# Optimization experiments

Measured on AMD Instinct MI355X. Metric: run time of the kernel, lower is better.

Reference implementation:

```python
import jax, jax.numpy as jnp
import numpy as np

B, C, N, H = 4, 256, 2048, 8
D = C // 4  # q/k projection dim
BN_EPS = 1e-5


def setup_inputs() -> dict:
    key = jax.random.key(0)
    ks = jax.random.split(key, 16)
    s = lambda fan: 1.0 / np.sqrt(fan)
    return {
        "x": jax.random.normal(ks[0], (B, C, N), dtype=jnp.float32),
        # per-head params, stacked on leading head axis
        "w_qk": jax.random.normal(ks[1], (H, D, C), dtype=jnp.float32) * s(C),  # shared q/k conv weight
        "w_v": jax.random.normal(ks[2], (H, C, C), dtype=jnp.float32) * s(C),
        "b_v": jax.random.normal(ks[3], (H, C), dtype=jnp.float32) * 0.01,
        "w_t": jax.random.normal(ks[4], (H, C, C), dtype=jnp.float32) * s(C),
        "b_t": jax.random.normal(ks[5], (H, C), dtype=jnp.float32) * 0.01,
        "bn_g": jnp.ones((H, C), dtype=jnp.float32),
        "bn_b": jnp.zeros((H, C), dtype=jnp.float32),
        "bn_m": jax.random.normal(ks[6], (H, C), dtype=jnp.float32) * 0.1,
        "bn_v": jax.random.uniform(ks[7], (H, C), dtype=jnp.float32, minval=0.5, maxval=1.5),
        # final 1x1 conv + BN (LeakyReLU 0.2)
        "w_lin": jax.random.normal(ks[8], (C, C * H), dtype=jnp.float32) * s(C * H),
        "lbn_g": jnp.ones((C,), dtype=jnp.float32),
        "lbn_b": jnp.zeros((C,), dtype=jnp.float32),
        "lbn_m": jax.random.normal(ks[9], (C,), dtype=jnp.float32) * 0.1,
        "lbn_v": jax.random.uniform(ks[10], (C,), dtype=jnp.float32, minval=0.5, maxval=1.5),
    }


def _oa_head(x, w_qk, w_v, b_v, w_t, b_t, g, b, m, v):
    # x: [B, C, N]; 1x1 Conv1d == channel matmul
    x_q = jnp.einsum("dc,bcn->bnd", w_qk, x)                 # [B, N, D]
    x_k = jnp.einsum("dc,bcn->bdn", w_qk, x)                 # [B, D, N] (shared weight)
    x_v = jnp.einsum("ec,bcn->ben", w_v, x) + b_v[:, None]   # [B, C, N]
    energy = jnp.einsum("bnd,bdm->bnm", x_q, x_k)            # [B, N, N]
    attn = jax.nn.softmax(energy, axis=-1)
    attn = attn / (1e-9 + attn.sum(axis=1, keepdims=True))   # extra L1 renorm over dim=1
    x_r = jnp.einsum("ben,bnm->bem", x_v, attn)              # [B, C, N]
    y = jnp.einsum("ec,bcn->ben", w_t, x - x_r) + b_t[:, None]
    y = (y - m[:, None]) * (g[:, None] / jnp.sqrt(v[:, None] + BN_EPS)) + b[:, None]
    return x + jax.nn.relu(y)


def reference(x, w_qk, w_v, b_v, w_t, b_t, bn_g, bn_b, bn_m, bn_v,
              w_lin, lbn_g, lbn_b, lbn_m, lbn_v):
    # run all H heads via vmap over stacked params -> [B, H, C, N]
    heads = jax.vmap(_oa_head, in_axes=(None, 0, 0, 0, 0, 0, 0, 0, 0, 0), out_axes=1)(
        x, w_qk, w_v, b_v, w_t, b_t, bn_g, bn_b, bn_m, bn_v)
    cat = heads.reshape(x.shape[0], H * C, x.shape[2])       # torch.cat(dim=1) order
    y = jnp.einsum("ck,bkn->bcn", w_lin, cat)                # 1x1 conv, no bias
    y = (y - lbn_m[:, None]) * (lbn_g[:, None] / jnp.sqrt(lbn_v[:, None] + BN_EPS)) + lbn_b[:, None]
    return jnp.where(y >= 0, y, 0.2 * y)                     # LeakyReLU(0.2)
```

## Files before the change

### kernel.cpp

```cpp
#include <hip/hip_runtime.h>
#include <math.h>

#define B_ 4
#define C_ 256
#define N_ 2048
#define H_ 8
#define D_ 64
#define BH_ 32
#define HC_ 2048
#define BN_EPS 1e-5f
#define SCL 1.2011224087864498f

typedef __attribute__((ext_vector_type(8))) short s8v;
typedef __attribute__((ext_vector_type(4))) short s4v;
typedef __attribute__((ext_vector_type(8))) _Float16 h8v;
typedef __attribute__((ext_vector_type(4))) _Float16 h4v;
typedef __attribute__((ext_vector_type(4))) float f32x4;

#define MFMA __builtin_amdgcn_mfma_f32_16x16x32_bf16
#define MFMAH __builtin_amdgcn_mfma_f32_16x16x32_f16

static __device__ __forceinline__ unsigned short f2b(float f) {
  union { float f; unsigned int i; } v; v.f = f;
  unsigned int r = v.i + 0x7FFFu + ((v.i >> 16) & 1u);
  return (unsigned short)(r >> 16);
}
static __device__ __forceinline__ float fexp2(float x) {
  float r;
  asm("v_exp_f32 %0, %1" : "=v"(r) : "v"(x));
  return r;
}
static __device__ __forceinline__ unsigned cvtpk(float lo, float hi) {
  unsigned r;
  asm("v_cvt_pk_bf16_f32 %0, %1, %2" : "=v"(r) : "v"(lo), "v"(hi));
  return r;
}
static __device__ __forceinline__ void gload16(const void* g, void* l) {
  __builtin_amdgcn_global_load_lds(
      (const __attribute__((address_space(1))) unsigned int*)g,
      (__attribute__((address_space(3))) unsigned int*)l, 16, 0, 0);
}

struct GP {
  const float *x, *w_qk, *w_v, *b_v, *w_t, *b_t, *bn_g, *bn_b, *bn_m, *bn_v;
  const float *w_lin, *lbn_g, *lbn_b, *lbn_m, *lbn_v;
  _Float16 *PT, *xT, *wqk16, *wvh;
  short *HOT, *wtb, *wlinb, *Vb, *xmr;
  float *part, *shb, *nrm, *sh, *out;
};

__global__ __launch_bounds__(256) void cvt_k(const float* __restrict__ in,
                                             short* __restrict__ out) {
  int i = (blockIdx.x * 256 + threadIdx.x) * 4;
  float4 v = *(const float4*)(in + i);
  s4v o = { (short)f2b(v.x), (short)f2b(v.y), (short)f2b(v.z), (short)f2b(v.w) };
  *(s4v*)(out + i) = o;
}

__global__ __launch_bounds__(256) void cvth_k(const float* __restrict__ in,
                                              _Float16* __restrict__ out) {
  int i = (blockIdx.x * 256 + threadIdx.x) * 4;
  float4 v = *(const float4*)(in + i);
  h4v o = { (_Float16)v.x, (_Float16)v.y, (_Float16)v.z, (_Float16)v.w };
  *(h4v*)(out + i) = o;
}

__global__ __launch_bounds__(256) void xcvt_k(const float* __restrict__ x,
                                              _Float16* __restrict__ xT) {
  const int n0 = blockIdx.x * 64, c0 = blockIdx.y * 64, b = blockIdx.z;
  const float* xb = x + (size_t)b * C_ * N_;
  __shared__ float sm[64][65];
  const int t = threadIdx.x;
#pragma unroll
  for (int i = 0; i < 4; ++i) {
    int idx = i * 256 + t;
    int c = idx >> 4, j = (idx & 15) * 4;
    float4 v = *(const float4*)(xb + (size_t)(c0 + c) * N_ + n0 + j);
    sm[j + 0][c] = v.x; sm[j + 1][c] = v.y; sm[j + 2][c] = v.z; sm[j + 3][c] = v.w;
  }
  __syncthreads();
#pragma unroll
  for (int i = 0; i < 2; ++i) {
    int idx = i * 256 + t;
    int n = idx >> 3, cg = (idx & 7) * 8;
    h8v o;
#pragma unroll
    for (int d = 0; d < 8; ++d) o[d] = (_Float16)sm[n][cg + d];
    *(h8v*)(xT + ((size_t)b * N_ + n0 + n) * C_ + c0 + cg) = o;
  }
}

__global__ __launch_bounds__(256, 2) void p_k(GP p) {
  const int t = threadIdx.x, wv = t >> 6, lane = t & 63;
  const int l15 = lane & 15, l4 = lane >> 4;
  const int n0 = blockIdx.x * 128;
  const int bh = blockIdx.y, b = bh / H_, h = bh % H_;
  const _Float16* Ag = p.wqk16 + h * D_ * C_;
  const _Float16* Bg = p.xT + (size_t)b * N_ * C_;
  __shared__ _Float16 As[64 * 64], Bs[128 * 64];
  __shared__ float Tr[128 * 65];
  f32x4 acc[4][2] = {};
  for (int kc = 0; kc < 256; kc += 64) {
    __syncthreads();
#pragma unroll
    for (int i = 0; i < 2; ++i) {
      int idx = i * 256 + t;
      int row = idx >> 3, offl = (idx & 7) * 16;
      gload16((const char*)(Ag + (size_t)row * C_ + kc) + (offl ^ ((row & 7) << 4)),
              (char*)As + idx * 16);
    }
#pragma unroll
    for (int i = 0; i < 4; ++i) {
      int idx = i * 256 + t;
      int row = idx >> 3, offl = (idx & 7) * 16;
      gload16((const char*)(Bg + (size_t)(n0 + row) * C_ + kc) + (offl ^ ((row & 7) << 4)),
              (char*)Bs + idx * 16);
    }
    __syncthreads();
    h8v ad[4][2], bn[2][2];
#pragma unroll
    for (int d = 0; d < 4; ++d)
#pragma unroll
      for (int ks = 0; ks < 2; ++ks) {
        int row = d * 16 + l15;
        ad[d][ks] = *(const h8v*)((const char*)As + row * 128 + ((ks * 64 + l4 * 16) ^ ((row & 7) << 4)));
      }
#pragma unroll
    for (int nb = 0; nb < 2; ++nb)
#pragma unroll
      for (int ks = 0; ks < 2; ++ks) {
        int row = wv * 32 + nb * 16 + l15;
        bn[nb][ks] = *(const h8v*)((const char*)Bs + row * 128 + ((ks * 64 + l4 * 16) ^ ((row & 7) << 4)));
      }
#pragma unroll
    for (int d = 0; d < 4; ++d)
#pragma unroll
      for (int nb = 0; nb < 2; ++nb) {
        acc[d][nb] = MFMAH(ad[d][0], bn[nb][0], acc[d][nb], 0, 0, 0);
        acc[d][nb] = MFMAH(ad[d][1], bn[nb][1], acc[d][nb], 0, 0, 0);
      }
  }
  __syncthreads();
#pragma unroll
  for (int d = 0; d < 4; ++d)
#pragma unroll
    for (int nb = 0; nb < 2; ++nb)
#pragma unroll
      for (int r = 0; r < 4; ++r) {
        int n_l = wv * 32 + nb * 16 + l15;
        int dd = d * 16 + l4 * 4 + r;
        Tr[n_l * 65 + dd] = acc[d][nb][r];
      }
  __syncthreads();
  _Float16* Pf = p.PT + ((size_t)bh * N_ + n0) * D_;
  float* nz = p.nrm + (size_t)bh * N_;
#pragma unroll
  for (int i = 0; i < 4; ++i) {
    int idx = i * 256 + t;
    int n = idx >> 3, dg = (idx & 7) * 8;
    h8v hv;
    float ssq = 0.f;
#pragma unroll
    for (int j = 0; j < 8; ++j) {
      float v = Tr[n * 65 + dg + j] * SCL;
      ssq = fmaf(v, v, ssq);
      hv[j] = (_Float16)v;
    }
    *(h8v*)(Pf + (size_t)n * D_ + dg) = hv;
    ssq += __shfl_xor(ssq, 1, 64);
    ssq += __shfl_xor(ssq, 2, 64);
    ssq += __shfl_xor(ssq, 4, 64);
    if ((t & 7) == 0) nz[n0 + n] = ssq;
  }
}

__global__ __launch_bounds__(256) void shift_k(const float* __restrict__ nrm,
                                               float* __restrict__ sh) {
  const int z = blockIdx.x, t = threadIdx.x;
  const float* nz = nrm + (size_t)z * N_;
  float loc[8];
  float mx = 0.f;
#pragma unroll
  for (int i = 0; i < 8; ++i) {
    loc[i] = nz[i * 256 + t];
    mx = fmaxf(mx, loc[i]);
  }
  for (int o = 32; o; o >>= 1) mx = fmaxf(mx, __shfl_xor(mx, o, 64));
  __shared__ float sb[4];
  if ((t & 63) == 0) sb[t >> 6] = mx;
  __syncthreads();
  float M = sqrtf(fmaxf(fmaxf(sb[0], sb[1]), fmaxf(sb[2], sb[3])));
#pragma unroll
  for (int i = 0; i < 8; ++i)
    sh[(size_t)z * N_ + i * 256 + t] = sqrtf(loc[i]) * M;
}

__global__ __launch_bounds__(256, 4) void passa_k(GP p) {
  const int t = threadIdx.x, wv = t >> 6, lane = t & 63;
  const int l15 = lane & 15, l4 = lane >> 4;
  const int wr = wv >> 1, wc = wv & 1;
  const int z = blockIdx.x;
  int idx = blockIdx.y;
  int ti = 0;
  while (idx >= 16 - ti) { idx -= 16 - ti; ++ti; }
  const int tj = ti + idx;
  const int r0 = ti * 128, c0 = tj * 128;
  const _Float16* Pz = p.PT + (size_t)z * N_ * D_;
  const float* shz = p.sh + (size_t)z * N_;
  __shared__ short RH[8192], CH[8192];
  __shared__ float rbuf[2][2][64], cbuf[2][2][64];
#pragma unroll
  for (int i = 0; i < 4; ++i) {
    int c2 = i * 256 + t;
    int row = c2 >> 3, offl = (c2 & 7) * 16;
    int so = offl ^ ((row & 7) << 4);
    gload16((const char*)(Pz + (size_t)(r0 + row) * D_) + so, (char*)RH + c2 * 16);
    if (ti != tj)
      gload16((const char*)(Pz + (size_t)(c0 + row) * D_) + so, (char*)CH + c2 * 16);
  }
  __syncthreads();
  const char* BHp = (ti == tj) ? (const char*)RH : (const char*)CH;

  h8v bh4[4][2];
  float shc[4];
#pragma unroll
  for (int nf = 0; nf < 4; ++nf) {
#pragma unroll
    for (int ks = 0; ks < 2; ++ks) {
      int row = wc * 64 + nf * 16 + l15;
      int byte = row * 128 + ((ks * 64 + l4 * 16) ^ ((row & 7) << 4));
      bh4[nf][ks] = *(const h8v*)(BHp + byte);
    }
    shc[nf] = shz[c0 + wc * 64 + nf * 16 + l15];
  }
  float rowp[4][4] = {};
  float colp[4] = {};
#pragma unroll
  for (int mf = 0; mf < 4; ++mf) {
    h8v ah[2];
#pragma unroll
    for (int ks = 0; ks < 2; ++ks) {
      int row = wr * 64 + mf * 16 + l15;
      int byte = row * 128 + ((ks * 64 + l4 * 16) ^ ((row & 7) << 4));
      ah[ks] = *(const h8v*)((const char*)RH + byte);
    }
    f32x4 shr = *(const f32x4*)(shz + r0 + wr * 64 + mf * 16 + l4 * 4);
#pragma unroll
    for (int nf = 0; nf < 4; ++nf) {
      f32x4 s = {};
      s = MFMAH(ah[0], bh4[nf][0], s, 0, 0, 0);
      s = MFMAH(ah[1], bh4[nf][1], s, 0, 0, 0);
      rowp[mf][0] += fexp2(s[0] - shr[0]);
      rowp[mf][1] += fexp2(s[1] - shr[1]);
      rowp[mf][2] += fexp2(s[2] - shr[2]);
      rowp[mf][3] += fexp2(s[3] - shr[3]);
      if (ti != tj)
        colp[nf] += fexp2(s[0] - shc[nf]) + fexp2(s[1] - shc[nf]) +
                    fexp2(s[2] - shc[nf]) + fexp2(s[3] - shc[nf]);
    }
  }
#pragma unroll
  for (int mf = 0; mf < 4; ++mf)
#pragma unroll
    for (int r = 0; r < 4; ++r) {
      float v = rowp[mf][r];
      v += __shfl_xor(v, 1, 64); v += __shfl_xor(v, 2, 64);
      v += __shfl_xor(v, 4, 64); v += __shfl_xor(v, 8, 64);
      rowp[mf][r] = v;
    }
#pragma unroll
  for (int nf = 0; nf < 4; ++nf) {
    float v = colp[nf];
    v += __shfl_xor(v, 16, 64); v += __shfl_xor(v, 32, 64);
    colp[nf] = v;
  }
  if (l15 == 0)
#pragma unroll
    for (int mf = 0; mf < 4; ++mf)
#pragma unroll
      for (int r = 0; r < 4; ++r)
        rbuf[wr][wc][mf * 16 + l4 * 4 + r] = rowp[mf][r];
  if (l4 == 0)
#pragma unroll
    for (int nf = 0; nf < 4; ++nf)
      cbuf[wc][wr][nf * 16 + l15] = colp[nf];
  __syncthreads();
  if (t < 128) {
    float v = rbuf[t >> 6][0][t & 63] + rbuf[t >> 6][1][t & 63];
    p.part[((size_t)z * 16 + tj) * N_ + r0 + t] = v;
  } else if (ti != tj) {
    int u = t - 128;
    float v = cbuf[u >> 6][0][u & 63] + cbuf[u >> 6][1][u & 63];
    p.part[((size_t)z * 16 + ti) * N_ + c0 + u] = v;
  }
}

__global__ __launch_bounds__(256) void shbred_k(const float* __restrict__ part,
                                                const float* __restrict__ sh,
                                                float* __restrict__ shb) {
  int i = blockIdx.x * 256 + threadIdx.x;
  int z = i >> 11, n = i & 2047;
  const float* pz = part + ((size_t)z * 16) * N_ + n;
  float s = 0.f;
#pragma unroll
  for (int j = 0; j < 16; ++j) s += pz[(size_t)j * N_];
  shb[i] = sh[i] + __log2f(s);
}

__global__ __launch_bounds__(256, 2) void passb_k(GP p) {
  const int t = threadIdx.x, wv = t >> 6, lane = t & 63;
  const int l15 = lane & 15, l4 = lane >> 4;
  const int z = blockIdx.x, b = z / H_;
  const int m0 = blockIdx.y * 128;
  const _Float16* Pz = p.PT + (size_t)z * N_ * D_;
  const short* Vz = p.Vb + (size_t)z * C_ * N_;
  const float* shbz = p.shb + (size_t)z * N_;

  __shared__ char smem[57856];
  float* cs_sm = (float*)(smem + 49152);
  float* shs = (float*)(smem + 49664);

  h8v bm[2][2];
#pragma unroll
  for (int mf = 0; mf < 2; ++mf)
#pragma unroll
    for (int ks = 0; ks < 2; ++ks)
      bm[mf][ks] = *(const h8v*)(Pz + (size_t)(m0 + wv * 32 + mf * 16 + l15) * D_ + ks * 32 + l4 * 8);

  s8v va[4][2];

#define STAGE_PN(n0v, bufbyte) do { \
    _Pragma("unroll") \
    for (int i_ = 0; i_ < 2; ++i_) { \
      int sl_ = i_ * 256 + t; \
      int rw_ = sl_ >> 3, of_ = (sl_ & 7) * 16; \
      gload16((const char*)(Pz + (size_t)((n0v) + rw_) * D_) + (of_ ^ ((rw_ & 7) << 4)), \
              smem + (bufbyte) + sl_ * 16); \
    } \
  } while (0)
#define ISSUE_V(n0v) do { \
    _Pragma("unroll") \
    for (int eb = 0; eb < 4; ++eb) { \
      const short* vr_ = Vz + (size_t)(wv * 64 + eb * 16 + l15) * N_ + (n0v) + l4 * 8; \
      va[eb][0] = *(const s8v*)vr_; \
      va[eb][1] = *(const s8v*)(vr_ + 32); \
    } \
  } while (0)

  f32x4 racc[4][8] = {};
  float csa0 = 0.f, csa1 = 0.f;

  STAGE_PN(0, 0);
  STAGE_PN(64, 8192);
  ISSUE_V(0);
#pragma unroll
  for (int i = 0; i < 2; ++i) {
    int ii = i * 256 + t;
    *(float4*)(shs + ii * 4) = *(const float4*)(shbz + ii * 4);
  }
  __syncthreads();

  for (int it = 0; it < 32; ++it) {
    const int n0 = it * 64;
    const int cur = it & 1;
    const char* PH = smem + cur * 8192;
    char* AT = smem + 16384 + cur * 16384;
#pragma unroll
    for (int nb = 0; nb < 4; ++nb) {
      int rowb = nb * 16 + l15;
      int sw = (rowb & 7) << 4;
      h8v an0 = *(const h8v*)(PH + rowb * 128 + ((l4 * 16) ^ sw));
      h8v an1 = *(const h8v*)(PH + rowb * 128 + ((64 + l4 * 16) ^ sw));
      f32x4 s0 = {}, s1 = {};
      s0 = MFMAH(an0, bm[0][0], s0, 0, 0, 0);
      s0 = MFMAH(an1, bm[0][1], s0, 0, 0, 0);
      s1 = MFMAH(an0, bm[1][0], s1, 0, 0, 0);
      s1 = MFMAH(an1, bm[1][1], s1, 0, 0, 0);
      f32x4 sb4 = *(const f32x4*)(shs + n0 + nb * 16 + l4 * 4);
      float a0 = fexp2(s0[0] - sb4[0]);
      float a1 = fexp2(s0[1] - sb4[1]);
      float a2 = fexp2(s0[2] - sb4[2]);
      float a3 = fexp2(s0[3] - sb4[3]);
      float c0 = fexp2(s1[0] - sb4[0]);
      float c1 = fexp2(s1[1] - sb4[1]);
      float c2 = fexp2(s1[2] - sb4[2]);
      float c3 = fexp2(s1[3] - sb4[3]);
      csa0 += (a0 + a1) + (a2 + a3);
      csa1 += (c0 + c1) + (c2 + c3);
      uint2 pk0 = { cvtpk(a0, a1), cvtpk(a2, a3) };
      uint2 pk1 = { cvtpk(c0, c1), cvtpk(c2, c3) };
      int swm = (l15 & 7) << 4;
      int cb = (nb * 32 + l4 * 8);
      *(uint2*)(AT + (wv * 32 + l15) * 128 + (cb ^ swm)) = pk0;
      *(uint2*)(AT + (wv * 32 + 16 + l15) * 128 + (cb ^ swm)) = pk1;
    }
    asm volatile("s_waitcnt vmcnt(8) lgkmcnt(0)" ::: "memory");
    __builtin_amdgcn_s_barrier();
    __builtin_amdgcn_sched_barrier(0);
    if (it < 30) STAGE_PN(n0 + 128, cur * 8192);
    __builtin_amdgcn_s_setprio(1);
#pragma unroll
    for (int mb = 0; mb < 8; ++mb) {
      int rowb = mb * 16 + l15;
      int sw = (rowb & 7) << 4;
      s8v at0 = *(const s8v*)(AT + rowb * 128 + ((l4 * 16) ^ sw));
      s8v at1 = *(const s8v*)(AT + rowb * 128 + ((64 + l4 * 16) ^ sw));
#pragma unroll
      for (int eb = 0; eb < 4; ++eb) {
        racc[eb][mb] = MFMA(va[eb][0], at0, racc[eb][mb], 0, 0, 0);
        racc[eb][mb] = MFMA(va[eb][1], at1, racc[eb][mb], 0, 0, 0);
      }
    }
    __builtin_amdgcn_s_setprio(0);
    if (it < 31) ISSUE_V(n0 + 64);
  }

  csa0 += __shfl_xor(csa0, 16, 64);
  csa0 += __shfl_xor(csa0, 32, 64);
  csa1 += __shfl_xor(csa1, 16, 64);
  csa1 += __shfl_xor(csa1, 32, 64);
  if (l4 == 0) {
    cs_sm[wv * 32 + l15] = csa0;
    cs_sm[wv * 32 + 16 + l15] = csa1;
  }
  __syncthreads();
  float invc[8];
#pragma unroll
  for (int mb = 0; mb < 8; ++mb) invc[mb] = 1.0f / (1e-9f + cs_sm[mb * 16 + l15]);
  const float* xb = p.x + (size_t)b * C_ * N_;
  char* Tr = smem;
#pragma unroll
  for (int half = 0; half < 2; ++half) {
    if (half) __syncthreads();
#pragma unroll
    for (int eb = 0; eb < 4; ++eb)
#pragma unroll
      for (int mbh = 0; mbh < 4; ++mbh) {
        int mb = half * 4 + mbh;
        int e0 = wv * 64 + eb * 16 + l4 * 4;
        int m_l = mbh * 16 + l15;
        int mg = m0 + mb * 16 + l15;
        float v0 = xb[(size_t)(e0 + 0) * N_ + mg] - racc[eb][mb][0] * invc[mb];
        float v1 = xb[(size_t)(e0 + 1) * N_ + mg] - racc[eb][mb][1] * invc[mb];
        float v2 = xb[(size_t)(e0 + 2) * N_ + mg] - racc[eb][mb][2] * invc[mb];
        float v3 = xb[(size_t)(e0 + 3) * N_ + mg] - racc[eb][mb][3] * invc[mb];
        uint2 pk = { cvtpk(v0, v1), cvtpk(v2, v3) };
        *(uint2*)(Tr + m_l * 512 + ((e0 * 2) ^ ((m_l & 7) << 4))) = pk;
      }
    __syncthreads();
    short* xz = p.xmr + ((size_t)z * N_ + m0 + half * 64) * C_;
#pragma unroll
    for (int i = 0; i < 8; ++i) {
      int idx = i * 256 + t;
      int m_l = idx >> 5, off2 = (idx & 31) * 16;
      s8v v = *(const s8v*)(Tr + m_l * 512 + (off2 ^ ((m_l & 7) << 4)));
      *(s8v*)((char*)(xz + (size_t)m_l * C_) + off2) = v;
    }
  }
#undef STAGE_PN
#undef ISSUE_V
}

template<int EPI>
__global__ __launch_bounds__(256) void mm_k(GP p) {
  constexpr int K = 256;
  const int t = threadIdx.x;
  const int wave = t >> 6, lane = t & 63;
  const int wr = wave >> 1, wc = wave & 1;
  const int l15 = lane & 15, l4 = lane >> 4;
  const int n0 = blockIdx.x * 128;
  const int m0 = blockIdx.y * 128;
  const int z = blockIdx.z;
  int b = z / H_, h = z % H_;

  const short *Ag, *Bg;
  if constexpr (EPI == 1) {
    Ag = (const short*)(p.wvh + (size_t)h * C_ * C_);
    Bg = (const short*)(p.xT + (size_t)b * N_ * C_);
  } else {
    Ag = p.wtb + (size_t)h * C_ * C_;
    Bg = p.xmr + (size_t)z * N_ * C_;
  }

  __shared__ short As[128 * 32];
  __shared__ short Bs[128 * 32];

  f32x4 acc[4][4] = {};

  for (int k0 = 0; k0 < K; k0 += 32) {
    __syncthreads();
#pragma unroll
    for (int i = 0; i < 2; ++i) {
      int idx = i * 256 + t;
      int row = idx >> 2, kg = (idx & 3) * 8;
      gload16(Ag + (size_t)(m0 + row) * K + k0 + kg, (char*)As + idx * 16);
      gload16(Bg + (size_t)(n0 + row) * K + k0 + kg, (char*)Bs + idx * 16);
    }
    __syncthreads();
    s8v af[4], bf[4];
#pragma unroll
    for (int m = 0; m < 4; ++m) af[m] = *(const s8v*)&As[(wr * 64 + m * 16 + l15) * 32 + l4 * 8];
#pragma unroll
    for (int n = 0; n < 4; ++n) bf[n] = *(const s8v*)&Bs[(wc * 64 + n * 16 + l15) * 32 + l4 * 8];
#pragma unroll
    for (int m = 0; m < 4; ++m)
#pragma unroll
      for (int n = 0; n < 4; ++n) {
        if constexpr (EPI == 1)
          acc[m][n] = MFMAH(__builtin_bit_cast(h8v, af[m]), __builtin_bit_cast(h8v, bf[n]),
                            acc[m][n], 0, 0, 0);
        else
          acc[m][n] = MFMA(af[m], bf[n], acc[m][n], 0, 0, 0);
      }
  }

  if constexpr (EPI == 1) {
    short* Vz = p.Vb + (size_t)z * C_ * N_;
#pragma unroll
    for (int m = 0; m < 4; ++m)
#pragma unroll
      for (int r = 0; r < 4; ++r) {
        int e = m0 + wr * 64 + m * 16 + l4 * 4 + r;
        float bias = p.b_v[h * C_ + e];
#pragma unroll
        for (int n = 0; n < 4; ++n) {
          int c = n0 + wc * 64 + n * 16 + l15;
          Vz[(size_t)e * N_ + c] = (short)f2b(acc[m][n][r] + bias);
        }
      }
  } else {
    __shared__ short Tr[128 * 128];
    const float* xb = p.x + (size_t)b * C_ * N_;
#pragma unroll
    for (int m = 0; m < 4; ++m)
#pragma unroll
      for (int r = 0; r < 4; ++r) {
        int e = m0 + wr * 64 + m * 16 + l4 * 4 + r;
        int el = e - m0;
        int hc = h * C_ + e;
        float bt = p.b_t[hc], mm = p.bn_m[hc], bb = p.bn_b[hc];
        float sc = p.bn_g[hc] / sqrtf(p.bn_v[hc] + BN_EPS);
#pragma unroll
        for (int n = 0; n < 4; ++n) {
          int cl = wc * 64 + n * 16 + l15;
          float y = (acc[m][n][r] + bt - mm) * sc + bb;
          float val = xb[(size_t)e * N_ + n0 + cl] + fmaxf(y, 0.f);
          Tr[cl * 128 + el] = (short)f2b(val);
        }
      }
    __syncthreads();
    short* Hz = p.HOT + (size_t)b * N_ * HC_;
#pragma unroll
    for (int it = 0; it < 8; ++it) {
      int idx = it * 256 + t;
      int cl = idx >> 4, eg = (idx & 15) * 8;
      *(s8v*)(Hz + (size_t)(n0 + cl) * HC_ + h * C_ + m0 + eg) = *(const s8v*)&Tr[cl * 128 + eg];
    }
  }
}

__global__ __launch_bounds__(256, 2) void mm4_k(GP p) {
  const int t = threadIdx.x, wv = t >> 6, lane = t & 63;
  const int l15 = lane & 15, l4 = lane >> 4;
  const int n0 = blockIdx.x * 128;
  const int m0 = blockIdx.y * 64;
  const int b = blockIdx.z;
  const short* Ag = p.wlinb;
  const short* Bg = p.HOT + (size_t)b * N_ * HC_;
  __shared__ short As[64 * 64], Bs[128 * 64];
  f32x4 acc[4][2] = {};
  for (int k0 = 0; k0 < HC_; k0 += 64) {
    __syncthreads();
#pragma unroll
    for (int i = 0; i < 2; ++i) {
      int sl = i * 256 + t;
      int rw = sl >> 3, of = (sl & 7) * 16;
      gload16((const char*)(Ag + (size_t)(m0 + rw) * HC_ + k0) + (of ^ ((rw & 7) << 4)),
              (char*)As + sl * 16);
    }
#pragma unroll
    for (int i = 0; i < 4; ++i) {
      int sl = i * 256 + t;
      int rw = sl >> 3, of = (sl & 7) * 16;
      gload16((const char*)(Bg + (size_t)(n0 + rw) * HC_ + k0) + (of ^ ((rw & 7) << 4)),
              (char*)Bs + sl * 16);
    }
    __syncthreads();
    s8v af[4][2], bf[2][2];
#pragma unroll
    for (int m = 0; m < 4; ++m)
#pragma unroll
      for (int ks = 0; ks < 2; ++ks) {
        int rw = m * 16 + l15;
        af[m][ks] = *(const s8v*)((const char*)As + rw * 128 + ((ks * 64 + l4 * 16) ^ ((rw & 7) << 4)));
      }
#pragma unroll
    for (int nf = 0; nf < 2; ++nf)
#pragma unroll
      for (int ks = 0; ks < 2; ++ks) {
        int rw = wv * 32 + nf * 16 + l15;
        bf[nf][ks] = *(const s8v*)((const char*)Bs + rw * 128 + ((ks * 64 + l4 * 16) ^ ((rw & 7) << 4)));
      }
#pragma unroll
    for (int m = 0; m < 4; ++m)
#pragma unroll
      for (int nf = 0; nf < 2; ++nf) {
        acc[m][nf] = MFMA(af[m][0], bf[nf][0], acc[m][nf], 0, 0, 0);
        acc[m][nf] = MFMA(af[m][1], bf[nf][1], acc[m][nf], 0, 0, 0);
      }
  }
  float* ob = p.out + (size_t)b * C_ * N_;
#pragma unroll
  for (int m = 0; m < 4; ++m)
#pragma unroll
    for (int r = 0; r < 4; ++r) {
      int e = m0 + m * 16 + l4 * 4 + r;
      float mm = p.lbn_m[e], bb = p.lbn_b[e];
      float sc = p.lbn_g[e] / sqrtf(p.lbn_v[e] + BN_EPS);
#pragma unroll
      for (int nf = 0; nf < 2; ++nf) {
        int c = n0 + wv * 32 + nf * 16 + l15;
        float y = (acc[m][nf][r] - mm) * sc + bb;
        ob[(size_t)e * N_ + c] = y >= 0.f ? y : 0.2f * y;
      }
    }
}

extern "C" void kernel_launch(void* const* d_in, const int* in_sizes, int n_in,
                              void* d_out, int out_size, void* d_ws, size_t ws_size,
                              hipStream_t stream) {
  GP p;
  p.x     = (const float*)d_in[0];
  p.w_qk  = (const float*)d_in[1];
  p.w_v   = (const float*)d_in[2];
  p.b_v   = (const float*)d_in[3];
  p.w_t   = (const float*)d_in[4];
  p.b_t   = (const float*)d_in[5];
  p.bn_g  = (const float*)d_in[6];
  p.bn_b  = (const float*)d_in[7];
  p.bn_m  = (const float*)d_in[8];
  p.bn_v  = (const float*)d_in[9];
  p.w_lin = (const float*)d_in[10];
  p.lbn_g = (const float*)d_in[11];
  p.lbn_b = (const float*)d_in[12];
  p.lbn_m = (const float*)d_in[13];
  p.lbn_v = (const float*)d_in[14];
  p.out   = (float*)d_out;

  char* base = (char*)d_ws;
  size_t off = 0;
  auto alloc = [&](size_t bytes) -> char* {
    char* r = base + off;
    off += (bytes + 255) & ~(size_t)255;
    return r;
  };
  p.PT    = (_Float16*)alloc((size_t)BH_ * N_ * D_ * 2);
  p.xT    = (_Float16*)alloc((size_t)B_ * N_ * C_ * 2);
  p.wqk16 = (_Float16*)alloc((size_t)H_ * D_ * C_ * 2);
  p.wvh   = (_Float16*)alloc((size_t)H_ * C_ * C_ * 2);
  p.wtb   = (short*)alloc((size_t)H_ * C_ * C_ * 2);
  p.wlinb = (short*)alloc((size_t)C_ * HC_ * 2);
  p.Vb    = (short*)alloc((size_t)BH_ * C_ * N_ * 2);
  p.xmr   = (short*)alloc((size_t)BH_ * N_ * C_ * 2);
  p.part  = (float*)alloc((size_t)BH_ * 16 * N_ * 4);
  p.shb   = (float*)alloc((size_t)BH_ * N_ * 4);
  p.nrm   = (float*)alloc((size_t)BH_ * N_ * 4);
  p.sh    = (float*)alloc((size_t)BH_ * N_ * 4);
  p.HOT   = p.Vb;

  dim3 blk(256);

  cvt_k<<<512, blk, 0, stream>>>(p.w_t, p.wtb);
  cvt_k<<<512, blk, 0, stream>>>(p.w_lin, p.wlinb);
  cvth_k<<<128, blk, 0, stream>>>(p.w_qk, p.wqk16);
  cvth_k<<<512, blk, 0, stream>>>(p.w_v, p.wvh);
  xcvt_k<<<dim3(32, 4, B_), blk, 0, stream>>>(p.x, p.xT);
  p_k<<<dim3(16, BH_), blk, 0, stream>>>(p);
  shift_k<<<BH_, blk, 0, stream>>>(p.nrm, p.sh);
  mm_k<1><<<dim3(16, 2, BH_), blk, 0, stream>>>(p);
  passa_k<<<dim3(32, 136), blk, 0, stream>>>(p);
  shbred_k<<<256, blk, 0, stream>>>(p.part, p.sh, p.shb);
  passb_k<<<dim3(32, 16), blk, 0, stream>>>(p);
  mm_k<3><<<dim3(16, 2, BH_), blk, 0, stream>>>(p);
  mm4_k<<<dim3(16, 4, B_), blk, 0, stream>>>(p);
}
```

Baseline: 228.8 us.

## Fuse weight conversions, double-buffer GEMM loads, single-buffer passb attention tile

Replaces four weight-conversion launches with one fused prep kernel. Adds double-buffered LDS prefetch of the next K-slice to mm_k and mm4_k so global loads overlap MFMA work, and raises mm4_k occupancy hint to 3. In passb_k, drops the double-buffered attention tile to shrink LDS so three blocks fit per CU, at the cost of an extra barrier per iteration.

After: 504.2 us. 120% more time.

```diff
diff --git a/kernel.cpp b/kernel.cpp
--- a/kernel.cpp
+++ b/kernel.cpp
@@ -49,20 +49,29 @@
   float *part, *shb, *nrm, *sh, *out;
 };
 
-__global__ __launch_bounds__(256) void cvt_k(const float* __restrict__ in,
-                                             short* __restrict__ out) {
-  int i = (blockIdx.x * 256 + threadIdx.x) * 4;
-  float4 v = *(const float4*)(in + i);
-  s4v o = { (short)f2b(v.x), (short)f2b(v.y), (short)f2b(v.z), (short)f2b(v.w) };
-  *(s4v*)(out + i) = o;
-}
-
-__global__ __launch_bounds__(256) void cvth_k(const float* __restrict__ in,
-                                              _Float16* __restrict__ out) {
-  int i = (blockIdx.x * 256 + threadIdx.x) * 4;
-  float4 v = *(const float4*)(in + i);
-  h4v o = { (_Float16)v.x, (_Float16)v.y, (_Float16)v.z, (_Float16)v.w };
-  *(h4v*)(out + i) = o;
+__global__ __launch_bounds__(256) void prep_k(GP p) {
+  int u = blockIdx.x * 256 + threadIdx.x;
+  if (u < 131072) {
+    int i = u * 4;
+    float4 v = *(const float4*)(p.w_t + i);
+    s4v o = { (short)f2b(v.x), (short)f2b(v.y), (short)f2b(v.z), (short)f2b(v.w) };
+    *(s4v*)(p.wtb + i) = o;
+  } else if (u < 262144) {
+    int i = (u - 131072) * 4;
+    float4 v = *(const float4*)(p.w_lin + i);
+    s4v o = { (short)f2b(v.x), (short)f2b(v.y), (short)f2b(v.z), (short)f2b(v.w) };
+    *(s4v*)(p.wlinb + i) = o;
+  } else if (u < 393216) {
+    int i = (u - 262144) * 4;
+    float4 v = *(const float4*)(p.w_v + i);
+    h4v o = { (_Float16)v.x, (_Float16)v.y, (_Float16)v.z, (_Float16)v.w };
+    *(h4v*)(p.wvh + i) = o;
+  } else {
+    int i = (u - 393216) * 4;
+    float4 v = *(const float4*)(p.w_qk + i);
+    h4v o = { (_Float16)v.x, (_Float16)v.y, (_Float16)v.z, (_Float16)v.w };
+    *(h4v*)(p.wqk16 + i) = o;
+  }
 }
 
 __global__ __launch_bounds__(256) void xcvt_k(const float* __restrict__ x,
@@ -307,7 +316,7 @@
   shb[i] = sh[i] + __log2f(s);
 }
 
-__global__ __launch_bounds__(256, 2) void passb_k(GP p) {
+__global__ __launch_bounds__(256, 3) void passb_k(GP p) {
   const int t = threadIdx.x, wv = t >> 6, lane = t & 63;
   const int l15 = lane & 15, l4 = lane >> 4;
   const int z = blockIdx.x, b = z / H_;
@@ -316,9 +325,10 @@
   const short* Vz = p.Vb + (size_t)z * C_ * N_;
   const float* shbz = p.shb + (size_t)z * N_;
 
-  __shared__ char smem[57856];
-  float* cs_sm = (float*)(smem + 49152);
-  float* shs = (float*)(smem + 49664);
+  __shared__ char smem[41472];
+  char* AT = smem + 16384;
+  float* cs_sm = (float*)(smem + 32768);
+  float* shs = (float*)(smem + 33280);
 
   h8v bm[2][2];
 #pragma unroll
@@ -362,9 +372,7 @@
 
   for (int it = 0; it < 32; ++it) {
     const int n0 = it * 64;
-    const int cur = it & 1;
-    const char* PH = smem + cur * 8192;
-    char* AT = smem + 16384 + cur * 16384;
+    const char* PH = smem + (it & 1) * 8192;
 #pragma unroll
     for (int nb = 0; nb < 4; ++nb) {
       int rowb = nb * 16 + l15;
@@ -397,7 +405,7 @@
     asm volatile("s_waitcnt vmcnt(8) lgkmcnt(0)" ::: "memory");
     __builtin_amdgcn_s_barrier();
     __builtin_amdgcn_sched_barrier(0);
-    if (it < 30) STAGE_PN(n0 + 128, cur * 8192);
+    if (it < 30) STAGE_PN(n0 + 128, (it & 1) * 8192);
     __builtin_amdgcn_s_setprio(1);
 #pragma unroll
     for (int mb = 0; mb < 8; ++mb) {
@@ -413,6 +421,9 @@
     }
     __builtin_amdgcn_s_setprio(0);
     if (it < 31) ISSUE_V(n0 + 64);
+    asm volatile("s_waitcnt lgkmcnt(0)" ::: "memory");
+    __builtin_amdgcn_s_barrier();
+    __builtin_amdgcn_sched_barrier(0);
   }
 
   csa0 += __shfl_xor(csa0, 16, 64);
@@ -482,26 +493,35 @@
     Bg = p.xmr + (size_t)z * N_ * C_;
   }
 
-  __shared__ short As[128 * 32];
-  __shared__ short Bs[128 * 32];
+  __shared__ short As[2][128 * 32];
+  __shared__ short Bs[2][128 * 32];
 
   f32x4 acc[4][4] = {};
 
-  for (int k0 = 0; k0 < K; k0 += 32) {
-    __syncthreads();
-#pragma unroll
-    for (int i = 0; i < 2; ++i) {
-      int idx = i * 256 + t;
-      int row = idx >> 2, kg = (idx & 3) * 8;
-      gload16(Ag + (size_t)(m0 + row) * K + k0 + kg, (char*)As + idx * 16);
-      gload16(Bg + (size_t)(n0 + row) * K + k0 + kg, (char*)Bs + idx * 16);
-    }
-    __syncthreads();
+#define STAGE_MM(ksv, bufv) do { \
+    int k0_ = (ksv) * 32; \
+    _Pragma("unroll") \
+    for (int i_ = 0; i_ < 2; ++i_) { \
+      int idx_ = i_ * 256 + t; \
+      int row_ = idx_ >> 2, kg_ = (idx_ & 3) * 8; \
+      gload16(Ag + (size_t)(m0 + row_) * K + k0_ + kg_, (char*)As[bufv] + idx_ * 16); \
+      gload16(Bg + (size_t)(n0 + row_) * K + k0_ + kg_, (char*)Bs[bufv] + idx_ * 16); \
+    } \
+  } while (0)
+
+  STAGE_MM(0, 0);
+  asm volatile("s_waitcnt vmcnt(0)" ::: "memory");
+  __builtin_amdgcn_s_barrier();
+  __builtin_amdgcn_sched_barrier(0);
+
+  for (int ks = 0; ks < 8; ++ks) {
+    const int cur = ks & 1;
+    if (ks < 7) STAGE_MM(ks + 1, cur ^ 1);
     s8v af[4], bf[4];
 #pragma unroll
-    for (int m = 0; m < 4; ++m) af[m] = *(const s8v*)&As[(wr * 64 + m * 16 + l15) * 32 + l4 * 8];
-#pragma unroll
-    for (int n = 0; n < 4; ++n) bf[n] = *(const s8v*)&Bs[(wc * 64 + n * 16 + l15) * 32 + l4 * 8];
+    for (int m = 0; m < 4; ++m) af[m] = *(const s8v*)&As[cur][(wr * 64 + m * 16 + l15) * 32 + l4 * 8];
+#pragma unroll
+    for (int n = 0; n < 4; ++n) bf[n] = *(const s8v*)&Bs[cur][(wc * 64 + n * 16 + l15) * 32 + l4 * 8];
 #pragma unroll
     for (int m = 0; m < 4; ++m)
 #pragma unroll
@@ -512,7 +532,11 @@
         else
           acc[m][n] = MFMA(af[m], bf[n], acc[m][n], 0, 0, 0);
       }
-  }
+    asm volatile("s_waitcnt vmcnt(0) lgkmcnt(0)" ::: "memory");
+    __builtin_amdgcn_s_barrier();
+    __builtin_amdgcn_sched_barrier(0);
+  }
+#undef STAGE_MM
 
   if constexpr (EPI == 1) {
     short* Vz = p.Vb + (size_t)z * C_ * N_;
@@ -559,7 +583,7 @@
   }
 }
 
-__global__ __launch_bounds__(256, 2) void mm4_k(GP p) {
+__global__ __launch_bounds__(256, 3) void mm4_k(GP p) {
   const int t = threadIdx.x, wv = t >> 6, lane = t & 63;
   const int l15 = lane & 15, l4 = lane >> 4;
   const int n0 = blockIdx.x * 128;
@@ -567,39 +591,48 @@
   const int b = blockIdx.z;
   const short* Ag = p.wlinb;
   const short* Bg = p.HOT + (size_t)b * N_ * HC_;
-  __shared__ short As[64 * 64], Bs[128 * 64];
+  __shared__ short As[2][64 * 64], Bs[2][128 * 64];
   f32x4 acc[4][2] = {};
-  for (int k0 = 0; k0 < HC_; k0 += 64) {
-    __syncthreads();
-#pragma unroll
-    for (int i = 0; i < 2; ++i) {
-      int sl = i * 256 + t;
-      int rw = sl >> 3, of = (sl & 7) * 16;
-      gload16((const char*)(Ag + (size_t)(m0 + rw) * HC_ + k0) + (of ^ ((rw & 7) << 4)),
-              (char*)As + sl * 16);
-    }
-#pragma unroll
-    for (int i = 0; i < 4; ++i) {
-      int sl = i * 256 + t;
-      int rw = sl >> 3, of = (sl & 7) * 16;
-      gload16((const char*)(Bg + (size_t)(n0 + rw) * HC_ + k0) + (of ^ ((rw & 7) << 4)),
-              (char*)Bs + sl * 16);
-    }
-    __syncthreads();
+
+#define STAGE_M4(k0v, bufv) do { \
+    _Pragma("unroll") \
+    for (int i_ = 0; i_ < 2; ++i_) { \
+      int sl_ = i_ * 256 + t; \
+      int rw_ = sl_ >> 3, of_ = (sl_ & 7) * 16; \
+      gload16((const char*)(Ag + (size_t)(m0 + rw_) * HC_ + (k0v)) + (of_ ^ ((rw_ & 7) << 4)), \
+              (char*)As[bufv] + sl_ * 16); \
+    } \
+    _Pragma("unroll") \
+    for (int i_ = 0; i_ < 4; ++i_) { \
+      int sl_ = i_ * 256 + t; \
+      int rw_ = sl_ >> 3, of_ = (sl_ & 7) * 16; \
+      gload16((const char*)(Bg + (size_t)(n0 + rw_) * HC_ + (k0v)) + (of_ ^ ((rw_ & 7) << 4)), \
+              (char*)Bs[bufv] + sl_ * 16); \
+    } \
+  } while (0)
+
+  STAGE_M4(0, 0);
+  asm volatile("s_waitcnt vmcnt(0)" ::: "memory");
+  __builtin_amdgcn_s_barrier();
+  __builtin_amdgcn_sched_barrier(0);
+
+  for (int ks = 0; ks < 32; ++ks) {
+    const int cur = ks & 1;
+    if (ks < 31) STAGE_M4((ks + 1) * 64, cur ^ 1);
     s8v af[4][2], bf[2][2];
 #pragma unroll
     for (int m = 0; m < 4; ++m)
 #pragma unroll
-      for (int ks = 0; ks < 2; ++ks) {
+      for (int k2 = 0; k2 < 2; ++k2) {
         int rw = m * 16 + l15;
-        af[m][ks] = *(const s8v*)((const char*)As + rw * 128 + ((ks * 64 + l4 * 16) ^ ((rw & 7) << 4)));
+        af[m][k2] = *(const s8v*)((const char*)As[cur] + rw * 128 + ((k2 * 64 + l4 * 16) ^ ((rw & 7) << 4)));
       }
 #pragma unroll
     for (int nf = 0; nf < 2; ++nf)
 #pragma unroll
-      for (int ks = 0; ks < 2; ++ks) {
+      for (int k2 = 0; k2 < 2; ++k2) {
         int rw = wv * 32 + nf * 16 + l15;
-        bf[nf][ks] = *(const s8v*)((const char*)Bs + rw * 128 + ((ks * 64 + l4 * 16) ^ ((rw & 7) << 4)));
+        bf[nf][k2] = *(const s8v*)((const char*)Bs[cur] + rw * 128 + ((k2 * 64 + l4 * 16) ^ ((rw & 7) << 4)));
       }
 #pragma unroll
     for (int m = 0; m < 4; ++m)
@@ -608,7 +641,12 @@
         acc[m][nf] = MFMA(af[m][0], bf[nf][0], acc[m][nf], 0, 0, 0);
         acc[m][nf] = MFMA(af[m][1], bf[nf][1], acc[m][nf], 0, 0, 0);
       }
-  }
+    asm volatile("s_waitcnt vmcnt(0) lgkmcnt(0)" ::: "memory");
+    __builtin_amdgcn_s_barrier();
+    __builtin_amdgcn_sched_barrier(0);
+  }
+#undef STAGE_M4
+
   float* ob = p.out + (size_t)b * C_ * N_;
 #pragma unroll
   for (int m = 0; m < 4; ++m)
@@ -670,10 +708,7 @@
 
   dim3 blk(256);
 
-  cvt_k<<<512, blk, 0, stream>>>(p.w_t, p.wtb);
-  cvt_k<<<512, blk, 0, stream>>>(p.w_lin, p.wlinb);
-  cvth_k<<<128, blk, 0, stream>>>(p.w_qk, p.wqk16);
-  cvth_k<<<512, blk, 0, stream>>>(p.w_v, p.wvh);
+  prep_k<<<1664, blk, 0, stream>>>(p);
   xcvt_k<<<dim3(32, 4, B_), blk, 0, stream>>>(p.x, p.xT);
   p_k<<<dim3(16, BH_), blk, 0, stream>>>(p);
   shift_k<<<BH_, blk, 0, stream>>>(p.nrm, p.sh);
```
